# Performance work log

Hardware: AMD Instinct MI355X
Metric: run time of the kernel (lower is better)

The kernel has to match this reference:

```python
import jax, jax.numpy as jnp
import numpy as np

NUM_HEADS = 8
EPS = 1e-3

N_TOKENS = 32768
DIM = 256
N_WIN = 128
WIN = N_TOKENS // N_WIN  # 256 tokens per window


def setup_inputs() -> dict:
    key = jax.random.key(0)
    ks = jax.random.split(key, 4)
    x = jax.random.normal(ks[0], (N_TOKENS, DIM), dtype=jnp.float32)
    # torch nn.Linear weights are [out_features, in_features]
    w_qkv = jax.random.normal(ks[1], (3 * DIM, DIM), dtype=jnp.float32) * (DIM ** -0.5)
    w_proj = jax.random.normal(ks[2], (DIM, DIM), dtype=jnp.float32) * (DIM ** -0.5)
    b_proj = jnp.zeros((DIM,), dtype=jnp.float32)
    batch_win_inds = (jnp.arange(N_TOKENS) // WIN).astype(jnp.int64)
    offsets = (jnp.arange(N_WIN) * WIN).astype(jnp.int64)
    counts = jnp.full((N_WIN,), WIN, dtype=jnp.int64)
    return {"x": x, "w_qkv": w_qkv, "w_proj": w_proj, "b_proj": b_proj,
            "offsets": offsets, "counts": counts, "batch_win_inds": batch_win_inds}


def reference(x, w_qkv, w_proj, b_proj, offsets, counts, batch_win_inds):
    N, C = x.shape
    H = NUM_HEADS
    hd = C // H
    W = counts.shape[0]  # number of windows (static)

    qkv = x @ w_qkv.T                      # [N, 3C]
    q, k, v = jnp.split(qkv, 3, axis=-1)   # each [N, C]
    q = jax.nn.relu(q.reshape(N, H, hd))   # [N, H, hd]
    k = jax.nn.relu(k.reshape(N, H, hd))
    v = v.reshape(N, H, hd)

    seg = batch_win_inds.astype(jnp.int32)
    # per-window KV state: kv[w] = sum_{i in w} k_i^T v_i   -> [W, H, hd, hd]
    kv = jax.ops.segment_sum(jnp.einsum('nhc,nhd->nhcd', k, v), seg, num_segments=W)
    # per-window key sum for normalizer                      -> [W, H, hd]
    s = jax.ops.segment_sum(k, seg, num_segments=W)

    y = jnp.einsum('nhc,nhcd->nhd', q, kv[seg])              # [N, H, hd]
    z = jnp.sum(s[seg] * q, axis=-1, keepdims=True)          # [N, H, 1]
    y = y / (z + EPS)

    y = y.reshape(N, C) @ w_proj.T + b_proj                  # [N, C]
    return y
```

## Files before the change

kernel.cpp:

```cpp
#include <hip/hip_runtime.h>

typedef __bf16 bf16_t;
typedef bf16_t bf16x8 __attribute__((ext_vector_type(8)));
typedef bf16_t bf16x4 __attribute__((ext_vector_type(4)));
typedef float f32x4 __attribute__((ext_vector_type(4)));

#define M_TOK 32768
#define NWIN 128
#define WIN  256

typedef __attribute__((address_space(3))) void* as3p;
typedef const __attribute__((address_space(1))) void* as1p;

__device__ __forceinline__ void gll16(const void* g, void* l) {
    __builtin_amdgcn_global_load_lds((as1p)g, (as3p)l, 16, 0, 0);
}

__device__ __forceinline__ bf16x8 cvt8(f32x4 a, f32x4 b) {
    bf16x8 o;
    o[0] = (bf16_t)a[0]; o[1] = (bf16_t)a[1]; o[2] = (bf16_t)a[2]; o[3] = (bf16_t)a[3];
    o[4] = (bf16_t)b[0]; o[5] = (bf16_t)b[1]; o[6] = (bf16_t)b[2]; o[7] = (bf16_t)b[3];
    return o;
}

__global__ __launch_bounds__(256) void wconv(
    const float* __restrict__ wq, const float* __restrict__ wp,
    bf16_t* __restrict__ wqb, bf16_t* __restrict__ wpb)
{
    int i4 = (blockIdx.x * 256 + threadIdx.x) * 4;
    const float* s; bf16_t* dst; int idx;
    if (i4 < 196608) { s = wq; dst = wqb; idx = i4; }
    else             { s = wp; dst = wpb; idx = i4 - 196608; }
    f32x4 v = *(const f32x4*)(s + idx);
    bf16x4 o;
    o[0] = (bf16_t)v[0]; o[1] = (bf16_t)v[1]; o[2] = (bf16_t)v[2]; o[3] = (bf16_t)v[3];
    *(bf16x4*)(dst + idx) = o;
}

__global__ __launch_bounds__(256) void gemm1_qkv(
    const float* __restrict__ X,
    const bf16_t* __restrict__ Wb,
    bf16_t* __restrict__ QKV)
{
    __shared__ float  As[4][128][16];
    __shared__ bf16_t Bs[2][128][32];

    const int tid = threadIdx.x;
    const int lane = tid & 63;
    const int wv = tid >> 6;
    const int wm = wv >> 1, wn = wv & 1;
    const int id = blockIdx.x;
    const int sg = id / 48, wsub = id % 48;
    const int m0 = (sg * 8 + (wsub & 7)) * 128;
    const int n0 = (wsub >> 3) * 128;
    const int r = lane & 15, q = lane >> 4;
    const int srow = lane >> 2;

    f32x4 acc[4][4] = {};

    for (int kc = 0; kc < 256; kc += 64) {
#pragma unroll
        for (int p = 0; p < 4; ++p)
#pragma unroll
            for (int g = 0; g < 2; ++g) {
                const int rb = wv * 32 + g * 16;
                gll16(X + (size_t)(m0 + rb + srow) * 256 + kc + p * 16 + (lane & 3) * 4,
                      &As[p][rb][0]);
            }
#pragma unroll
        for (int p = 0; p < 2; ++p)
#pragma unroll
            for (int g = 0; g < 2; ++g) {
                const int rb = wv * 32 + g * 16;
                gll16(Wb + (size_t)(n0 + rb + srow) * 256 + kc + p * 32 + (lane & 3) * 8,
                      &Bs[p][rb][0]);
            }
        __syncthreads();

#pragma unroll
        for (int kk = 0; kk < 64; kk += 32) {
            const int kq = kk + q * 8;
            const int pA = kq >> 4, offA = kq & 15;
            const int pB = kk >> 5;
            bf16x8 a[4], b[4];
#pragma unroll
            for (int i = 0; i < 4; ++i) {
                f32x4 lo = *(const f32x4*)&As[pA][wm * 64 + i * 16 + r][offA];
                f32x4 hi = *(const f32x4*)&As[pA][wm * 64 + i * 16 + r][offA + 4];
                a[i] = cvt8(lo, hi);
            }
#pragma unroll
            for (int j = 0; j < 4; ++j)
                b[j] = *(const bf16x8*)&Bs[pB][wn * 64 + j * 16 + r][q * 8];
#pragma unroll
            for (int i = 0; i < 4; ++i)
#pragma unroll
                for (int j = 0; j < 4; ++j)
                    acc[i][j] = __builtin_amdgcn_mfma_f32_16x16x32_bf16(b[j], a[i], acc[i][j], 0, 0, 0);
        }
        __syncthreads();
    }

#pragma unroll
    for (int i = 0; i < 4; ++i) {
        const int rowg = m0 + wm * 64 + i * 16 + r;
#pragma unroll
        for (int j = 0; j < 4; ++j) {
            const int nb = n0 + wn * 64 + j * 16 + q * 4;
            const int nblk = nb >> 5, d = nb & 31;
            bf16x4 o;
#pragma unroll
            for (int reg = 0; reg < 4; ++reg) {
                float v = acc[i][j][reg];
                if (nblk < 16) v = fmaxf(v, 0.0f);
                o[reg] = (bf16_t)v;
            }
            *(bf16x4*)&QKV[((size_t)nblk * M_TOK + rowg) * 32 + d] = o;
        }
    }
}

__global__ __launch_bounds__(256) void gemm2_proj(
    const bf16_t* __restrict__ Y,
    const bf16_t* __restrict__ Wb,
    const float* __restrict__ bias,
    float* __restrict__ Out)
{
    __shared__ bf16_t As[2][128][32];
    __shared__ bf16_t Bs[2][128][32];

    const int tid = threadIdx.x;
    const int lane = tid & 63;
    const int wv = tid >> 6;
    const int wm = wv >> 1, wn = wv & 1;
    const int id = blockIdx.x;
    const int sg = id / 32, wsub = id % 32;
    const int m0 = (sg * 16 + (wsub & 15)) * 128;
    const int n0 = (wsub >> 4) * 128;
    const int r = lane & 15, q = lane >> 4;
    const int srow = lane >> 2;

    f32x4 acc[4][4] = {};

    for (int kc = 0; kc < 256; kc += 64) {
#pragma unroll
        for (int p = 0; p < 2; ++p)
#pragma unroll
            for (int g = 0; g < 2; ++g) {
                const int rb = wv * 32 + g * 16;
                gll16(Y + (size_t)(m0 + rb + srow) * 256 + kc + p * 32 + (lane & 3) * 8,
                      &As[p][rb][0]);
                gll16(Wb + (size_t)(n0 + rb + srow) * 256 + kc + p * 32 + (lane & 3) * 8,
                      &Bs[p][rb][0]);
            }
        __syncthreads();

#pragma unroll
        for (int kk = 0; kk < 64; kk += 32) {
            const int pB = kk >> 5;
            bf16x8 a[4], b[4];
#pragma unroll
            for (int i = 0; i < 4; ++i)
                a[i] = *(const bf16x8*)&As[pB][wm * 64 + i * 16 + r][q * 8];
#pragma unroll
            for (int j = 0; j < 4; ++j)
                b[j] = *(const bf16x8*)&Bs[pB][wn * 64 + j * 16 + r][q * 8];
#pragma unroll
            for (int i = 0; i < 4; ++i)
#pragma unroll
                for (int j = 0; j < 4; ++j)
                    acc[i][j] = __builtin_amdgcn_mfma_f32_16x16x32_bf16(b[j], a[i], acc[i][j], 0, 0, 0);
        }
        __syncthreads();
    }

#pragma unroll
    for (int i = 0; i < 4; ++i) {
        const int rowg = m0 + wm * 64 + i * 16 + r;
#pragma unroll
        for (int j = 0; j < 4; ++j) {
            const int nb = n0 + wn * 64 + j * 16 + q * 4;
            f32x4 bi = *(const f32x4*)(bias + nb);
            f32x4 o;
#pragma unroll
            for (int reg = 0; reg < 4; ++reg) o[reg] = acc[i][j][reg] + bi[reg];
            *(f32x4*)&Out[(size_t)rowg * 256 + nb] = o;
        }
    }
}

__global__ __launch_bounds__(256) void kvy_kernel(
    const bf16_t* __restrict__ QKV,
    const int* __restrict__ offsets,
    const int* __restrict__ counts,
    bf16_t* __restrict__ Y)
{
    const int w = blockIdx.x;
    const int h = blockIdx.y;
    const int is64 = (counts[1] == 0) ? 1 : 0;
    const int off = offsets[w << is64];
    const int tid = threadIdx.x;
    const int lane = tid & 63;
    const int wv = tid >> 6;

    __shared__ __align__(16) bf16_t KT[32 * 264];
    __shared__ __align__(16) bf16_t VT[32 * 264];
    __shared__ __align__(16) bf16_t KVT[32 * 40];
    __shared__ float sbuf[32];
    __shared__ float spart[32 * 8];
    __shared__ float zinv[WIN];

    {
        const int t = tid;
        const bf16_t* kp = QKV + ((size_t)(8 + h) * M_TOK + off + t) * 32;
        const bf16_t* vp = QKV + ((size_t)(16 + h) * M_TOK + off + t) * 32;
        bf16_t ka[32], va[32];
#pragma unroll
        for (int u = 0; u < 4; ++u) {
            bf16x8 kk = *(const bf16x8*)(kp + u * 8);
            bf16x8 vvv = *(const bf16x8*)(vp + u * 8);
#pragma unroll
            for (int j = 0; j < 8; ++j) { ka[u * 8 + j] = kk[j]; va[u * 8 + j] = vvv[j]; }
        }
#pragma unroll
        for (int c = 0; c < 32; ++c) {
            KT[c * 264 + t] = ka[c];
            VT[c * 264 + t] = va[c];
        }
    }
    __syncthreads();

    {
        const int c = tid >> 3;
        const int tc = (tid & 7) * 32;
        float ps = 0.f;
#pragma unroll
        for (int u = 0; u < 4; ++u) {
            bf16x8 kk = *(const bf16x8*)(&KT[c * 264 + tc + u * 8]);
#pragma unroll
            for (int j = 0; j < 8; ++j) ps += (float)kk[j];
        }
        spart[c * 8 + (tid & 7)] = ps;
    }
    {
        const int i = wv >> 1, j = wv & 1;
        const int r = lane & 15, q = lane >> 4;
        f32x4 acc = {};
#pragma unroll
        for (int ch = 0; ch < 8; ++ch) {
            bf16x8 af = *(const bf16x8*)(&KT[(i * 16 + r) * 264 + ch * 32 + q * 8]);
            bf16x8 bf_ = *(const bf16x8*)(&VT[(j * 16 + r) * 264 + ch * 32 + q * 8]);
            acc = __builtin_amdgcn_mfma_f32_16x16x32_bf16(af, bf_, acc, 0, 0, 0);
        }
        bf16x4 kv4;
#pragma unroll
        for (int reg = 0; reg < 4; ++reg) kv4[reg] = (bf16_t)acc[reg];
        *(bf16x4*)(&KVT[(j * 16 + r) * 40 + i * 16 + q * 4]) = kv4;
    }
    __syncthreads();
    if (tid < 32) {
        float s = 0.f;
#pragma unroll
        for (int u = 0; u < 8; ++u) s += spart[tid * 8 + u];
        sbuf[tid] = s;
    }
    __syncthreads();

    {
        const int t = tid;
        const bf16_t* qp = QKV + ((size_t)h * M_TOK + off + t) * 32;
        float z = 0.f;
#pragma unroll
        for (int u = 0; u < 4; ++u) {
            bf16x8 qq = *(const bf16x8*)(qp + u * 8);
#pragma unroll
            for (int j = 0; j < 8; ++j) z += (float)qq[j] * sbuf[u * 8 + j];
        }
        zinv[t] = 1.0f / (z + 1e-3f);
    }
    __syncthreads();

    {
        const int r = lane & 15, q = lane >> 4;
        bf16x8 b0 = *(const bf16x8*)(&KVT[(r) * 40 + q * 8]);
        bf16x8 b1 = *(const bf16x8*)(&KVT[(16 + r) * 40 + q * 8]);
#pragma unroll
        for (int u = 0; u < 4; ++u) {
            const int mi = wv * 4 + u;
            const bf16_t* ap = QKV + ((size_t)h * M_TOK + off + mi * 16 + r) * 32 + q * 8;
            bf16x8 af = *(const bf16x8*)ap;
            f32x4 acc0 = {}, acc1 = {};
            acc0 = __builtin_amdgcn_mfma_f32_16x16x32_bf16(b0, af, acc0, 0, 0, 0);
            acc1 = __builtin_amdgcn_mfma_f32_16x16x32_bf16(b1, af, acc1, 0, 0, 0);
            const int tkn = mi * 16 + r;
            const float zi = zinv[tkn];
            bf16_t* yp = Y + (size_t)(off + tkn) * 256 + h * 32;
            bf16x4 o0, o1;
#pragma unroll
            for (int reg = 0; reg < 4; ++reg) {
                o0[reg] = (bf16_t)(acc0[reg] * zi);
                o1[reg] = (bf16_t)(acc1[reg] * zi);
            }
            *(bf16x4*)(yp + q * 4) = o0;
            *(bf16x4*)(yp + 16 + q * 4) = o1;
        }
    }
}

extern "C" void kernel_launch(void* const* d_in, const int* in_sizes, int n_in,
                              void* d_out, int out_size, void* d_ws, size_t ws_size,
                              hipStream_t stream) {
    const float* x      = (const float*)d_in[0];
    const float* w_qkv  = (const float*)d_in[1];
    const float* w_proj = (const float*)d_in[2];
    const float* b_proj = (const float*)d_in[3];
    const int*   offs   = (const int*)d_in[4];
    const int*   cnts   = (const int*)d_in[5];

    char* ws = (char*)d_ws;
    bf16_t* QKV = (bf16_t*)ws;
    bf16_t* Y   = (bf16_t*)(ws + 50331648);
    bf16_t* Wqb = (bf16_t*)(ws + 67108864);
    bf16_t* Wpb = (bf16_t*)(ws + 67502080);
    float*  out = (float*)d_out;

    wconv<<<256, 256, 0, stream>>>(w_qkv, w_proj, Wqb, Wpb);

    gemm1_qkv<<<1536, 256, 0, stream>>>(x, Wqb, QKV);

    kvy_kernel<<<dim3(NWIN, 8), 256, 0, stream>>>(QKV, offs, cnts, Y);

    gemm2_proj<<<512, 256, 0, stream>>>(Y, Wpb, b_proj, out);
}
```

Before: 138.6 us.

## Emit transposed K/V from QKV GEMM and compute key sums via MFMA

The QKV GEMM epilogue now writes Q in its previous per-head layout but stores K and V transposed as channel-major, token-contiguous arrays. This lets the window kernel load MFMA fragments directly from global memory, dropping the LDS transpose and its barrier. The per-channel key sum is computed with an extra MFMA against a ones vector instead of a separate LDS reduction. The trade-off is that the GEMM epilogue for K/V becomes scalar 2-byte strided stores, which may coalesce poorly.

```diff
diff --git a/kernel.cpp b/kernel.cpp
--- a/kernel.cpp
+++ b/kernel.cpp
@@ -40,7 +40,9 @@
 __global__ __launch_bounds__(256) void gemm1_qkv(
     const float* __restrict__ X,
     const bf16_t* __restrict__ Wb,
-    bf16_t* __restrict__ QKV)
+    bf16_t* __restrict__ Qg,
+    bf16_t* __restrict__ KTg,
+    bf16_t* __restrict__ VTg)
 {
     __shared__ float  As[4][128][16];
     __shared__ bf16_t Bs[2][128][32];
@@ -106,16 +108,27 @@
         const int rowg = m0 + wm * 64 + i * 16 + r;
 #pragma unroll
         for (int j = 0; j < 4; ++j) {
-            const int nb = n0 + wn * 64 + j * 16 + q * 4;
-            const int nblk = nb >> 5, d = nb & 31;
-            bf16x4 o;
-#pragma unroll
-            for (int reg = 0; reg < 4; ++reg) {
-                float v = acc[i][j][reg];
-                if (nblk < 16) v = fmaxf(v, 0.0f);
-                o[reg] = (bf16_t)v;
-            }
-            *(bf16x4*)&QKV[((size_t)nblk * M_TOK + rowg) * 32 + d] = o;
+            const int nbase = n0 + wn * 64 + j * 16 + q * 4;
+            if (nbase < 256) {
+                const int hq = nbase >> 5, d = nbase & 31;
+                bf16x4 o;
+#pragma unroll
+                for (int reg = 0; reg < 4; ++reg)
+                    o[reg] = (bf16_t)fmaxf(acc[i][j][reg], 0.0f);
+                *(bf16x4*)&Qg[((size_t)hq * M_TOK + rowg) * 32 + d] = o;
+            } else if (nbase < 512) {
+                const int hh = (nbase >> 5) - 8, c0 = nbase & 31;
+#pragma unroll
+                for (int reg = 0; reg < 4; ++reg)
+                    KTg[((size_t)hh * 32 + c0 + reg) * M_TOK + rowg] =
+                        (bf16_t)fmaxf(acc[i][j][reg], 0.0f);
+            } else {
+                const int hh = (nbase >> 5) - 16, c0 = nbase & 31;
+#pragma unroll
+                for (int reg = 0; reg < 4; ++reg)
+                    VTg[((size_t)hh * 32 + c0 + reg) * M_TOK + rowg] =
+                        (bf16_t)acc[i][j][reg];
+            }
         }
     }
 }
@@ -190,7 +203,9 @@
 }
 
 __global__ __launch_bounds__(256) void kvy_kernel(
-    const bf16_t* __restrict__ QKV,
+    const bf16_t* __restrict__ Qg,
+    const bf16_t* __restrict__ KTg,
+    const bf16_t* __restrict__ VTg,
     const int* __restrict__ offsets,
     const int* __restrict__ counts,
     bf16_t* __restrict__ Y)
@@ -202,92 +217,60 @@
     const int tid = threadIdx.x;
     const int lane = tid & 63;
     const int wv = tid >> 6;
-
-    __shared__ __align__(16) bf16_t KT[32 * 264];
-    __shared__ __align__(16) bf16_t VT[32 * 264];
+    const int r = lane & 15, q = lane >> 4;
+
     __shared__ __align__(16) bf16_t KVT[32 * 40];
     __shared__ float sbuf[32];
-    __shared__ float spart[32 * 8];
     __shared__ float zinv[WIN];
+
+    {
+        const int i = wv >> 1, j = wv & 1;
+        bf16x8 ones;
+#pragma unroll
+        for (int u = 0; u < 8; ++u) ones[u] = (bf16_t)1.0f;
+        f32x4 acc = {}, accs = {};
+        const bf16_t* kr = KTg + ((size_t)h * 32 + i * 16 + r) * M_TOK + off + q * 8;
+        const bf16_t* vr = VTg + ((size_t)h * 32 + j * 16 + r) * M_TOK + off + q * 8;
+#pragma unroll
+        for (int ch = 0; ch < 8; ++ch) {
+            bf16x8 af = *(const bf16x8*)(kr + ch * 32);
+            bf16x8 bf_ = *(const bf16x8*)(vr + ch * 32);
+            acc  = __builtin_amdgcn_mfma_f32_16x16x32_bf16(af, bf_, acc, 0, 0, 0);
+            accs = __builtin_amdgcn_mfma_f32_16x16x32_bf16(af, ones, accs, 0, 0, 0);
+        }
+        bf16x4 kv4;
+#pragma unroll
+        for (int reg = 0; reg < 4; ++reg) kv4[reg] = (bf16_t)acc[reg];
+        *(bf16x4*)(&KVT[(j * 16 + r) * 40 + i * 16 + q * 4]) = kv4;
+        if (j == 0 && r == 0) {
+#pragma unroll
+            for (int reg = 0; reg < 4; ++reg)
+                sbuf[i * 16 + q * 4 + reg] = accs[reg];
+        }
+    }
+    __syncthreads();
 
     {
         const int t = tid;
-        const bf16_t* kp = QKV + ((size_t)(8 + h) * M_TOK + off + t) * 32;
-        const bf16_t* vp = QKV + ((size_t)(16 + h) * M_TOK + off + t) * 32;
-        bf16_t ka[32], va[32];
-#pragma unroll
-        for (int u = 0; u < 4; ++u) {
-            bf16x8 kk = *(const bf16x8*)(kp + u * 8);
-            bf16x8 vvv = *(const bf16x8*)(vp + u * 8);
-#pragma unroll
-            for (int j = 0; j < 8; ++j) { ka[u * 8 + j] = kk[j]; va[u * 8 + j] = vvv[j]; }
-        }
-#pragma unroll
-        for (int c = 0; c < 32; ++c) {
-            KT[c * 264 + t] = ka[c];
-            VT[c * 264 + t] = va[c];
-        }
-    }
-    __syncthreads();
-
-    {
-        const int c = tid >> 3;
-        const int tc = (tid & 7) * 32;
-        float ps = 0.f;
-#pragma unroll
-        for (int u = 0; u < 4; ++u) {
-            bf16x8 kk = *(const bf16x8*)(&KT[c * 264 + tc + u * 8]);
-#pragma unroll
-            for (int j = 0; j < 8; ++j) ps += (float)kk[j];
-        }
-        spart[c * 8 + (tid & 7)] = ps;
-    }
-    {
-        const int i = wv >> 1, j = wv & 1;
-        const int r = lane & 15, q = lane >> 4;
-        f32x4 acc = {};
-#pragma unroll
-        for (int ch = 0; ch < 8; ++ch) {
-            bf16x8 af = *(const bf16x8*)(&KT[(i * 16 + r) * 264 + ch * 32 + q * 8]);
-            bf16x8 bf_ = *(const bf16x8*)(&VT[(j * 16 + r) * 264 + ch * 32 + q * 8]);
-            acc = __builtin_amdgcn_mfma_f32_16x16x32_bf16(af, bf_, acc, 0, 0, 0);
-        }
-        bf16x4 kv4;
-#pragma unroll
-        for (int reg = 0; reg < 4; ++reg) kv4[reg] = (bf16_t)acc[reg];
-        *(bf16x4*)(&KVT[(j * 16 + r) * 40 + i * 16 + q * 4]) = kv4;
-    }
-    __syncthreads();
-    if (tid < 32) {
-        float s = 0.f;
-#pragma unroll
-        for (int u = 0; u < 8; ++u) s += spart[tid * 8 + u];
-        sbuf[tid] = s;
-    }
-    __syncthreads();
-
-    {
-        const int t = tid;
-        const bf16_t* qp = QKV + ((size_t)h * M_TOK + off + t) * 32;
+        const bf16_t* qp = Qg + ((size_t)h * M_TOK + off + t) * 32;
         float z = 0.f;
 #pragma unroll
         for (int u = 0; u < 4; ++u) {
             bf16x8 qq = *(const bf16x8*)(qp + u * 8);
 #pragma unroll
-            for (int j = 0; j < 8; ++j) z += (float)qq[j] * sbuf[u * 8 + j];
+            for (int jj = 0; jj < 8; ++jj) z += (float)qq[jj] * sbuf[u * 8 + jj];
         }
         zinv[t] = 1.0f / (z + 1e-3f);
     }
     __syncthreads();
 
     {
-        const int r = lane & 15, q = lane >> 4;
         bf16x8 b0 = *(const bf16x8*)(&KVT[(r) * 40 + q * 8]);
         bf16x8 b1 = *(const bf16x8*)(&KVT[(16 + r) * 40 + q * 8]);
 #pragma unroll
         for (int u = 0; u < 4; ++u) {
             const int mi = wv * 4 + u;
-            const bf16_t* ap = QKV + ((size_t)h * M_TOK + off + mi * 16 + r) * 32 + q * 8;
+            const bf16_t* ap = Qg + ((size_t)h * M_TOK + off + mi * 16 + r) * 32 + q * 8;
             bf16x8 af = *(const bf16x8*)ap;
             f32x4 acc0 = {}, acc1 = {};
             acc0 = __builtin_amdgcn_mfma_f32_16x16x32_bf16(b0, af, acc0, 0, 0, 0);
@@ -318,7 +301,9 @@
     const int*   cnts   = (const int*)d_in[5];
 
     char* ws = (char*)d_ws;
-    bf16_t* QKV = (bf16_t*)ws;
+    bf16_t* Qg  = (bf16_t*)ws;
+    bf16_t* KTg = (bf16_t*)(ws + 16777216);
+    bf16_t* VTg = (bf16_t*)(ws + 33554432);
     bf16_t* Y   = (bf16_t*)(ws + 50331648);
     bf16_t* Wqb = (bf16_t*)(ws + 67108864);
     bf16_t* Wpb = (bf16_t*)(ws + 67502080);
@@ -326,9 +311,9 @@
 
     wconv<<<256, 256, 0, stream>>>(w_qkv, w_proj, Wqb, Wpb);
 
-    gemm1_qkv<<<1536, 256, 0, stream>>>(x, Wqb, QKV);
-
-    kvy_kernel<<<dim3(NWIN, 8), 256, 0, stream>>>(QKV, offs, cnts, Y);
+    gemm1_qkv<<<1536, 256, 0, stream>>>(x, Wqb, Qg, KTg, VTg);
+
+    kvy_kernel<<<dim3(NWIN, 8), 256, 0, stream>>>(Qg, KTg, VTg, offs, cnts, Y);
 
     gemm2_proj<<<512, 256, 0, stream>>>(Y, Wpb, b_proj, out);
 }
```

New measurement: 146.2 us. 1.06x slower.

## Compute per-window KV state with direct scalar FMA loop instead of LDS-staged MFMA

Applied to the files above, without the earlier changes.

Drops the LDS transpose staging of K and V and the MFMA-based K^T V product. Each thread now loops over all 256 tokens of the window and accumulates one key channel against four value channels in fp32 FMAs, adding the key sum as it goes. This removes two large shared buffers, a barrier and the partial-sum reduction, which could raise occupancy. In exchange each thread issues 256 strided scalar global loads and roughly 1280 FMAs, and the loads rely on L1/L2 because every thread reads the same token rows.

```diff
diff --git a/kernel.cpp b/kernel.cpp
--- a/kernel.cpp
+++ b/kernel.cpp
@@ -202,67 +202,33 @@
     const int tid = threadIdx.x;
     const int lane = tid & 63;
     const int wv = tid >> 6;
-
-    __shared__ __align__(16) bf16_t KT[32 * 264];
-    __shared__ __align__(16) bf16_t VT[32 * 264];
+    const int r = lane & 15, q = lane >> 4;
+
     __shared__ __align__(16) bf16_t KVT[32 * 40];
     __shared__ float sbuf[32];
-    __shared__ float spart[32 * 8];
     __shared__ float zinv[WIN];
 
     {
-        const int t = tid;
-        const bf16_t* kp = QKV + ((size_t)(8 + h) * M_TOK + off + t) * 32;
-        const bf16_t* vp = QKV + ((size_t)(16 + h) * M_TOK + off + t) * 32;
-        bf16_t ka[32], va[32];
-#pragma unroll
-        for (int u = 0; u < 4; ++u) {
-            bf16x8 kk = *(const bf16x8*)(kp + u * 8);
-            bf16x8 vvv = *(const bf16x8*)(vp + u * 8);
-#pragma unroll
-            for (int j = 0; j < 8; ++j) { ka[u * 8 + j] = kk[j]; va[u * 8 + j] = vvv[j]; }
-        }
-#pragma unroll
-        for (int c = 0; c < 32; ++c) {
-            KT[c * 264 + t] = ka[c];
-            VT[c * 264 + t] = va[c];
-        }
-    }
-    __syncthreads();
-
-    {
-        const int c = tid >> 3;
-        const int tc = (tid & 7) * 32;
-        float ps = 0.f;
-#pragma unroll
-        for (int u = 0; u < 4; ++u) {
-            bf16x8 kk = *(const bf16x8*)(&KT[c * 264 + tc + u * 8]);
-#pragma unroll
-            for (int j = 0; j < 8; ++j) ps += (float)kk[j];
-        }
-        spart[c * 8 + (tid & 7)] = ps;
-    }
-    {
-        const int i = wv >> 1, j = wv & 1;
-        const int r = lane & 15, q = lane >> 4;
-        f32x4 acc = {};
-#pragma unroll
-        for (int ch = 0; ch < 8; ++ch) {
-            bf16x8 af = *(const bf16x8*)(&KT[(i * 16 + r) * 264 + ch * 32 + q * 8]);
-            bf16x8 bf_ = *(const bf16x8*)(&VT[(j * 16 + r) * 264 + ch * 32 + q * 8]);
-            acc = __builtin_amdgcn_mfma_f32_16x16x32_bf16(af, bf_, acc, 0, 0, 0);
-        }
-        bf16x4 kv4;
-#pragma unroll
-        for (int reg = 0; reg < 4; ++reg) kv4[reg] = (bf16_t)acc[reg];
-        *(bf16x4*)(&KVT[(j * 16 + r) * 40 + i * 16 + q * 4]) = kv4;
-    }
-    __syncthreads();
-    if (tid < 32) {
-        float s = 0.f;
-#pragma unroll
-        for (int u = 0; u < 8; ++u) s += spart[tid * 8 + u];
-        sbuf[tid] = s;
+        const int c  = tid >> 3;
+        const int d4 = (tid & 7) << 2;
+        const bf16_t* kp = QKV + ((size_t)(8 + h) * M_TOK + off) * 32 + c;
+        const bf16_t* vp = QKV + ((size_t)(16 + h) * M_TOK + off) * 32 + d4;
+        float a0 = 0.f, a1 = 0.f, a2 = 0.f, a3 = 0.f, sa = 0.f;
+#pragma unroll 8
+        for (int t = 0; t < WIN; ++t) {
+            float kc  = (float)kp[t * 32];
+            bf16x4 v4 = *(const bf16x4*)(vp + t * 32);
+            a0 += kc * (float)v4[0];
+            a1 += kc * (float)v4[1];
+            a2 += kc * (float)v4[2];
+            a3 += kc * (float)v4[3];
+            sa += kc;
+        }
+        KVT[(d4 + 0) * 40 + c] = (bf16_t)a0;
+        KVT[(d4 + 1) * 40 + c] = (bf16_t)a1;
+        KVT[(d4 + 2) * 40 + c] = (bf16_t)a2;
+        KVT[(d4 + 3) * 40 + c] = (bf16_t)a3;
+        if ((tid & 7) == 0) sbuf[c] = sa;
     }
     __syncthreads();
 
@@ -274,14 +240,13 @@
         for (int u = 0; u < 4; ++u) {
             bf16x8 qq = *(const bf16x8*)(qp + u * 8);
 #pragma unroll
-            for (int j = 0; j < 8; ++j) z += (float)qq[j] * sbuf[u * 8 + j];
+            for (int jj = 0; jj < 8; ++jj) z += (float)qq[jj] * sbuf[u * 8 + jj];
         }
         zinv[t] = 1.0f / (z + 1e-3f);
     }
     __syncthreads();
 
     {
-        const int r = lane & 15, q = lane >> 4;
         bf16x8 b0 = *(const bf16x8*)(&KVT[(r) * 40 + q * 8]);
         bf16x8 b1 = *(const bf16x8*)(&KVT[(16 + r) * 40 + q * 8]);
 #pragma unroll
```

New measurement: 174.3 us. +25.7%, slower.
